# Kernel optimization log

Measured on AMD Instinct MI355X. Metric: run time of the kernel, lower is better.

The kernel has to match this reference:

```python
import jax, jax.numpy as jnp
import numpy as np

CUTOFF = 1.6  # short_range_cutoff from init_kwargs
E = 20_000_000
N_ATOMS = 100_000


def setup_inputs() -> dict:
    key = jax.random.key(0)
    k1, k2, k3 = jax.random.split(key, 3)
    Rij = jax.random.normal(k1, (E, 3), dtype=jnp.float32)
    idx_i = jax.random.randint(k2, (E,), 0, N_ATOMS, dtype=jnp.int32)
    idx_j = jax.random.randint(k3, (E,), 0, N_ATOMS, dtype=jnp.int32)
    return {"Rij": Rij, "idx_i": idx_i, "idx_j": idx_j}


def reference(Rij, idx_i, idx_j):
    """Faithful jit-compatible version of FilterShortRange.forward.

    torch.nonzero produces a dynamic-size index list; under jit we use the
    static-size equivalent jnp.nonzero(size=E, fill_value=0) and a validity
    mask: the first n_sr entries of the compacted outputs are exactly the
    short-range edges (same order as torch), padding beyond n_sr is zeroed
    (indices set to -1).
    """
    rij = jnp.linalg.norm(Rij, axis=-1)              # [E] per-edge distance
    mask = rij <= CUTOFF                             # [E] bool
    n_sr = jnp.sum(mask)                             # number of short-range edges
    (cidx,) = jnp.nonzero(mask, size=E, fill_value=0)  # stable compaction indices
    valid = jnpp_arange(E) < n_sr if False else (jnp.arange(E) < n_sr)  # [E]
    Rij_sr = jnp.where(valid[:, None], Rij[cidx], 0.0)   # [E,3], first n_sr rows valid
    idx_i_sr = jnp.where(valid, idx_i[cidx], -1)
    idx_j_sr = jnp.where(valid, idx_j[cidx], -1)
    # (Rij_lr, idx_i_lr, idx_j_lr, Rij, idx_i, idx_j, count)
    return (Rij, idx_i, idx_j, Rij_sr, idx_i_sr, idx_j_sr, n_sr)
```

## Files before the change

### kernel.cpp

```cpp
#include <hip/hip_runtime.h>

#define CUTOFF 1.6f
#define BLOCK 256
#define EPT 8
#define EPB (BLOCK * EPT)

typedef float f32x4 __attribute__((ext_vector_type(4)));

__global__ void __launch_bounds__(BLOCK) k1_count_copy(
    const float* __restrict__ Rij, float* __restrict__ outRij,
    int* __restrict__ counts, long E)
{
  long b = blockIdx.x;
  int t = threadIdx.x;
  long base = b * (long)EPB + (long)t * EPT;
  int cnt = 0;
  if (base < E) {
    const f32x4* rp4 = (const f32x4*)(Rij + base * 3);
    f32x4* op4 = (f32x4*)(outRij + base * 3);
    float rr[24];
#pragma unroll
    for (int q = 0; q < 6; ++q) {
      f32x4 v = rp4[q];
      op4[q] = v;
      rr[4 * q + 0] = v.x; rr[4 * q + 1] = v.y;
      rr[4 * q + 2] = v.z; rr[4 * q + 3] = v.w;
    }
#pragma unroll
    for (int k = 0; k < EPT; ++k) {
      float x = rr[3 * k], y = rr[3 * k + 1], z = rr[3 * k + 2];
      float s = sqrtf(x * x + y * y + z * z);
      cnt += (s <= CUTOFF) ? 1 : 0;
    }
  }
#pragma unroll
  for (int d = 32; d > 0; d >>= 1) cnt += __shfl_down(cnt, d, 64);
  __shared__ int ssum;
  if (t == 0) ssum = 0;
  __syncthreads();
  if ((t & 63) == 0) atomicAdd(&ssum, cnt);
  __syncthreads();
  if (t == 0) counts[b] = ssum;
}

__global__ void __launch_bounds__(1024) k2_scan(
    int* __restrict__ counts, int nb, int* __restrict__ nsr,
    float* __restrict__ out_nsr)
{
  int t = threadIdx.x;
  int C = (nb + 1023) >> 10;
  int start = t * C;
  int end = min(start + C, nb);
  int sum = 0;
  for (int i = start; i < end; ++i) sum += counts[i];
  int lane = t & 63, wid = t >> 6;
  int v = sum;
#pragma unroll
  for (int d = 1; d < 64; d <<= 1) {
    int n = __shfl_up(v, d, 64);
    if (lane >= d) v += n;
  }
  __shared__ int wsum[16];
  if (lane == 63) wsum[wid] = v;
  __syncthreads();
  int woff = 0;
  for (int w = 0; w < wid; ++w) woff += wsum[w];
  int run = woff + v - sum;
  for (int i = start; i < end; ++i) {
    int c = counts[i];
    counts[i] = run;
    run += c;
  }
  if (t == 1023) {
    nsr[0] = run;
    out_nsr[0] = (float)run;
  }
}

__global__ void __launch_bounds__(BLOCK) k3_scatter_fill(
    const float* __restrict__ Rij, const int* __restrict__ idx_i,
    const int* __restrict__ idx_j, const int* __restrict__ offs,
    const int* __restrict__ nsr, float* __restrict__ out, long E, int nb)
{
  long b = blockIdx.x;
  int t = threadIdx.x;
  int lane = t & 63, wid = t >> 6;
  long base = b * (long)EPB + (long)t * EPT;
  long n = nsr[0];

  float rr[24];
  int ii[EPT], jj[EPT];
  unsigned m = 0;
  int cnt = 0;
  if (base < E) {
    const f32x4* rp4 = (const f32x4*)(Rij + base * 3);
#pragma unroll
    for (int q = 0; q < 6; ++q) {
      f32x4 v = rp4[q];
      rr[4 * q + 0] = v.x; rr[4 * q + 1] = v.y;
      rr[4 * q + 2] = v.z; rr[4 * q + 3] = v.w;
    }
    const int4* ip = (const int4*)(idx_i + base);
    const int4* jp = (const int4*)(idx_j + base);
    int4 ia = ip[0], ib = ip[1], ja = jp[0], jb = jp[1];
    ii[0] = ia.x; ii[1] = ia.y; ii[2] = ia.z; ii[3] = ia.w;
    ii[4] = ib.x; ii[5] = ib.y; ii[6] = ib.z; ii[7] = ib.w;
    jj[0] = ja.x; jj[1] = ja.y; jj[2] = ja.z; jj[3] = ja.w;
    jj[4] = jb.x; jj[5] = jb.y; jj[6] = jb.z; jj[7] = jb.w;
    f32x4 fi0 = {(float)ii[0], (float)ii[1], (float)ii[2], (float)ii[3]};
    f32x4 fi1 = {(float)ii[4], (float)ii[5], (float)ii[6], (float)ii[7]};
    f32x4 fj0 = {(float)jj[0], (float)jj[1], (float)jj[2], (float)jj[3]};
    f32x4 fj1 = {(float)jj[4], (float)jj[5], (float)jj[6], (float)jj[7]};
    *(f32x4*)(out + 3 * E + base) = fi0;
    *(f32x4*)(out + 3 * E + base + 4) = fi1;
    *(f32x4*)(out + 4 * E + base) = fj0;
    *(f32x4*)(out + 4 * E + base + 4) = fj1;
#pragma unroll
    for (int k = 0; k < EPT; ++k) {
      float x = rr[3 * k], y = rr[3 * k + 1], z = rr[3 * k + 2];
      float s = sqrtf(x * x + y * y + z * z);
      if (s <= CUTOFF) { m |= 1u << k; ++cnt; }
    }
  }

  int sv = cnt;
#pragma unroll
  for (int d = 1; d < 64; d <<= 1) {
    int nn = __shfl_up(sv, d, 64);
    if (lane >= d) sv += nn;
  }
  __shared__ int wsum[BLOCK / 64];
  if (lane == 63) wsum[wid] = sv;
  __syncthreads();
  int woff = 0;
#pragma unroll
  for (int w = 0; w < BLOCK / 64; ++w)
    if (w < wid) woff += wsum[w];
  long pos = (long)offs[b] + woff + (sv - cnt);

  if (base < E && m) {
    float* srf = out + 5 * E;
    float* oi = out + 8 * E;
    float* oj = out + 9 * E;
#pragma unroll
    for (int k = 0; k < EPT; ++k) {
      if (m & (1u << k)) {
        srf[3 * pos + 0] = rr[3 * k + 0];
        srf[3 * pos + 1] = rr[3 * k + 1];
        srf[3 * pos + 2] = rr[3 * k + 2];
        oi[pos] = (float)ii[k];
        oj[pos] = (float)jj[k];
        ++pos;
      }
    }
  }

  {
    long len = 3 * (E - n);
    long share = (len + nb - 1) / nb;
    long lo = 5 * E + 3 * n + b * share;
    long hi = lo + share;
    long cap = 8 * E;
    if (hi > cap) hi = cap;
    for (long i = lo + t; i < hi; i += BLOCK) out[i] = 0.0f;
  }
  {
    long len = E - n;
    long share = (len + nb - 1) / nb;
    long lo = 8 * E + n + b * share;
    long hi = lo + share;
    long cap = 9 * E;
    if (hi > cap) hi = cap;
    for (long i = lo + t; i < hi; i += BLOCK) out[i] = -1.0f;
  }
  {
    long len = E - n;
    long share = (len + nb - 1) / nb;
    long lo = 9 * E + n + b * share;
    long hi = lo + share;
    long cap = 10 * E;
    if (hi > cap) hi = cap;
    for (long i = lo + t; i < hi; i += BLOCK) out[i] = -1.0f;
  }
}

extern "C" void kernel_launch(void* const* d_in, const int* in_sizes, int n_in,
                              void* d_out, int out_size, void* d_ws,
                              size_t ws_size, hipStream_t stream)
{
  const float* Rij = (const float*)d_in[0];
  const int* idx_i = (const int*)d_in[1];
  const int* idx_j = (const int*)d_in[2];
  long E = (long)in_sizes[1];
  float* out = (float*)d_out;

  int nb = (int)((E + EPB - 1) / EPB);
  int* counts = (int*)d_ws;
  int* nsr = counts + nb;

  k1_count_copy<<<nb, BLOCK, 0, stream>>>(Rij, out, counts, E);
  k2_scan<<<1, 1024, 0, stream>>>(counts, nb, nsr, out + 10 * E);
  k3_scatter_fill<<<nb, BLOCK, 0, stream>>>(Rij, idx_i, idx_j, counts, nsr,
                                            out, E, nb);
}
```

Before: 348.1 us.

## Stage compacted edges in LDS and write them out with coalesced vector stores

```diff
diff --git a/kernel.cpp b/kernel.cpp
--- a/kernel.cpp
+++ b/kernel.cpp
@@ -77,6 +77,43 @@
   }
 }
 
+__device__ __forceinline__ void coop_copy(float* __restrict__ dst,
+                                          const float* __restrict__ src,
+                                          int len, int t)
+{
+  int h = (int)(((16u - (unsigned)((unsigned long long)dst & 15ull)) >> 2) & 3u);
+  if (h > len) h = len;
+  if (t < h) dst[t] = src[t];
+  int n4 = (len - h) >> 2;
+  f32x4* d4 = (f32x4*)(dst + h);
+  for (int q = t; q < n4; q += BLOCK) {
+    int s = h + 4 * q;
+    f32x4 v = {src[s], src[s + 1], src[s + 2], src[s + 3]};
+    d4[q] = v;
+  }
+  int done = h + 4 * n4;
+  int rem = len - done;
+  if (t < rem) dst[done + t] = src[done + t];
+}
+
+__device__ __forceinline__ void coop_fill(float* __restrict__ base, long lo,
+                                          long hi, float val, int t)
+{
+  long len = hi - lo;
+  if (len <= 0) return;
+  float* p = base + lo;
+  int h = (int)(((16u - (unsigned)((unsigned long long)p & 15ull)) >> 2) & 3u);
+  if ((long)h > len) h = (int)len;
+  if (t < h) p[t] = val;
+  long n4 = (len - h) >> 2;
+  f32x4* d4 = (f32x4*)(p + h);
+  f32x4 v = {val, val, val, val};
+  for (long q = t; q < n4; q += BLOCK) d4[q] = v;
+  long done = h + 4 * n4;
+  int rem = (int)(len - done);
+  if (t < rem) p[done + t] = val;
+}
+
 __global__ void __launch_bounds__(BLOCK) k3_scatter_fill(
     const float* __restrict__ Rij, const int* __restrict__ idx_i,
     const int* __restrict__ idx_j, const int* __restrict__ offs,
@@ -87,6 +124,11 @@
   int lane = t & 63, wid = t >> 6;
   long base = b * (long)EPB + (long)t * EPT;
   long n = nsr[0];
+
+  __shared__ float sR[3 * EPB];
+  __shared__ float sI[EPB];
+  __shared__ float sJ[EPB];
+  __shared__ int wsum[BLOCK / 64];
 
   float rr[24];
   int ii[EPT], jj[EPT];
@@ -129,58 +171,64 @@
     int nn = __shfl_up(sv, d, 64);
     if (lane >= d) sv += nn;
   }
-  __shared__ int wsum[BLOCK / 64];
   if (lane == 63) wsum[wid] = sv;
   __syncthreads();
-  int woff = 0;
-#pragma unroll
-  for (int w = 0; w < BLOCK / 64; ++w)
-    if (w < wid) woff += wsum[w];
-  long pos = (long)offs[b] + woff + (sv - cnt);
+  int woff = 0, bsum = 0;
+#pragma unroll
+  for (int w = 0; w < BLOCK / 64; ++w) {
+    int s = wsum[w];
+    if (w < wid) woff += s;
+    bsum += s;
+  }
+  int texcl = woff + sv - cnt;
 
   if (base < E && m) {
-    float* srf = out + 5 * E;
-    float* oi = out + 8 * E;
-    float* oj = out + 9 * E;
+    int p = texcl;
 #pragma unroll
     for (int k = 0; k < EPT; ++k) {
       if (m & (1u << k)) {
-        srf[3 * pos + 0] = rr[3 * k + 0];
-        srf[3 * pos + 1] = rr[3 * k + 1];
-        srf[3 * pos + 2] = rr[3 * k + 2];
-        oi[pos] = (float)ii[k];
-        oj[pos] = (float)jj[k];
-        ++pos;
+        sR[3 * p + 0] = rr[3 * k + 0];
+        sR[3 * p + 1] = rr[3 * k + 1];
+        sR[3 * p + 2] = rr[3 * k + 2];
+        sI[p] = (float)ii[k];
+        sJ[p] = (float)jj[k];
+        ++p;
       }
     }
   }
+  __syncthreads();
+
+  long off = offs[b];
+  coop_copy(out + 5 * E + 3 * off, sR, 3 * bsum, t);
+  coop_copy(out + 8 * E + off, sI, bsum, t);
+  coop_copy(out + 9 * E + off, sJ, bsum, t);
 
   {
     long len = 3 * (E - n);
-    long share = (len + nb - 1) / nb;
+    long share = ((len + nb - 1) / nb + 3) & ~3L;
     long lo = 5 * E + 3 * n + b * share;
     long hi = lo + share;
     long cap = 8 * E;
     if (hi > cap) hi = cap;
-    for (long i = lo + t; i < hi; i += BLOCK) out[i] = 0.0f;
+    coop_fill(out, lo, hi, 0.0f, t);
   }
   {
     long len = E - n;
-    long share = (len + nb - 1) / nb;
+    long share = ((len + nb - 1) / nb + 3) & ~3L;
     long lo = 8 * E + n + b * share;
     long hi = lo + share;
     long cap = 9 * E;
     if (hi > cap) hi = cap;
-    for (long i = lo + t; i < hi; i += BLOCK) out[i] = -1.0f;
+    coop_fill(out, lo, hi, -1.0f, t);
   }
   {
     long len = E - n;
-    long share = (len + nb - 1) / nb;
+    long share = ((len + nb - 1) / nb + 3) & ~3L;
     long lo = 9 * E + n + b * share;
     long hi = lo + share;
     long cap = 10 * E;
     if (hi > cap) hi = cap;
-    for (long i = lo + t; i < hi; i += BLOCK) out[i] = -1.0f;
+    coop_fill(out, lo, hi, -1.0f, t);
   }
 }
 
```

After: 305.1 us. 1.14x faster.
